# Kernel optimization log

Hardware: AMD Instinct MI355X
Metric: run time of the kernel (lower is better)

The kernel has to match this reference:

```python
import jax, jax.numpy as jnp
import numpy as np

N = 100000   # total nodes
E = 1000000  # edges
D = 64       # input_dim
H = 128      # embed_dim


def setup_inputs() -> dict:
    key = jax.random.key(0)
    k1, k2, k3, k4 = jax.random.split(key, 4)
    nodes = jnp.arange(N, dtype=jnp.int32)
    features = jax.random.normal(k1, (N, D), dtype=jnp.float32)
    edge_index = jax.random.randint(k2, (2, E), 0, N, dtype=jnp.int32)
    # nn.Linear(2*D, H): weight [H, 2D], bias [H]
    W = jax.random.normal(k3, (H, 2 * D), dtype=jnp.float32) / np.sqrt(2 * D)
    b = jax.random.normal(k4, (H,), dtype=jnp.float32) * 0.01
    return {"nodes": nodes, "features": features, "edge_index": edge_index,
            "W": W, "b": b}


def reference(nodes, features, edge_index, W, b):
    src, dst = edge_index[0], edge_index[1]
    # gcn=False: neighbors are undirected (both src->dst and dst->src).
    # Mean aggregator over all neighbors (full-neighborhood mean).
    ones = jnp.ones((E,), dtype=features.dtype)
    neigh_sum = (jax.ops.segment_sum(features[dst], src, num_segments=N)
                 + jax.ops.segment_sum(features[src], dst, num_segments=N))
    deg = (jax.ops.segment_sum(ones, src, num_segments=N)
           + jax.ops.segment_sum(ones, dst, num_segments=N))
    neigh_mean = neigh_sum / jnp.maximum(deg, 1.0)[:, None]  # [N, D]
    self_feats = features[nodes]            # [B, D]
    neigh_feats = neigh_mean[nodes]         # [B, D]
    combined = jnp.concatenate([self_feats, neigh_feats], axis=1)  # [B, 2D]
    out = jax.nn.relu(combined @ W.T + b)   # [B, H]
    return out
```

## Files before the change

### kernel.cpp

```cpp
#include <hip/hip_runtime.h>
#include <hip/hip_bf16.h>


#define D_IN 64
#define H_OUT 128
#define CAP 64
#define CAP_L 61
#define NPB 32
#define BSHIFT 8
#define BUK_N 256
#define NBUK_MAX 512
#define PASSA_BLOCKS 256
#define PASSA_THREADS 512

typedef unsigned long long ull;
typedef unsigned short ushortt;
typedef unsigned char uchar;
typedef __attribute__((ext_vector_type(8))) short bf16x8;
typedef __attribute__((ext_vector_type(4))) float f32x4;
typedef __attribute__((ext_vector_type(2))) float f32x2;

__device__ __forceinline__ ushortt f2bf(float f) {
    __hip_bfloat16 h = __float2bfloat16(f);
    return *reinterpret_cast<ushortt*>(&h);
}
__device__ __forceinline__ float bf2f(ushortt u) {
    unsigned int x = ((unsigned int)u) << 16;
    return __uint_as_float(x);
}

__global__ __launch_bounds__(PASSA_THREADS) void prep_kernel(
    const int* __restrict__ ei,
    unsigned* __restrict__ gbuf,
    int* __restrict__ blkcnt,
    const float4* __restrict__ feat4,
    const float4* __restrict__ w4,
    ushortt* __restrict__ fb,
    uint2* __restrict__ fq,
    ushortt* __restrict__ Wb,
    int E, int nbuk, int scap, int chunk, int nfeat8, int nw8)
{
    const int t = threadIdx.x;

    if (blockIdx.x >= PASSA_BLOCKS) {
        int i = (blockIdx.x - PASSA_BLOCKS) * PASSA_THREADS + t;
        if (i < nfeat8) {
            float4 a = feat4[2 * i], b = feat4[2 * i + 1];
            bf16x8 o;
            o[0] = (short)f2bf(a.x); o[1] = (short)f2bf(a.y);
            o[2] = (short)f2bf(a.z); o[3] = (short)f2bf(a.w);
            o[4] = (short)f2bf(b.x); o[5] = (short)f2bf(b.y);
            o[6] = (short)f2bf(b.z); o[7] = (short)f2bf(b.w);
            *(bf16x8*)&fb[(size_t)i * 8] = o;
            unsigned lo = (unsigned)__builtin_amdgcn_cvt_pk_fp8_f32(a.x, a.y, 0, false);
            lo = (unsigned)__builtin_amdgcn_cvt_pk_fp8_f32(a.z, a.w, (int)lo, true);
            unsigned hi = (unsigned)__builtin_amdgcn_cvt_pk_fp8_f32(b.x, b.y, 0, false);
            hi = (unsigned)__builtin_amdgcn_cvt_pk_fp8_f32(b.z, b.w, (int)hi, true);
            uint2 q; q.x = lo; q.y = hi;
            fq[i] = q;
        } else {
            int j = i - nfeat8;
            if (j < nw8) {
                float4 a = w4[2 * j], b = w4[2 * j + 1];
                bf16x8 o;
                o[0] = (short)f2bf(a.x); o[1] = (short)f2bf(a.y);
                o[2] = (short)f2bf(a.z); o[3] = (short)f2bf(a.w);
                o[4] = (short)f2bf(b.x); o[5] = (short)f2bf(b.y);
                o[6] = (short)f2bf(b.z); o[7] = (short)f2bf(b.w);
                *(bf16x8*)&Wb[(size_t)j * 8] = o;
            }
        }
        return;
    }

    __shared__ int lcnt[NBUK_MAX];
    for (int i = t; i < nbuk; i += PASSA_THREADS) lcnt[i] = 0;
    __syncthreads();

    const int E2 = 2 * E;
    int lo = blockIdx.x * chunk;
    int hi = lo + chunk; if (hi > E2) hi = E2;

    for (int i = lo + t; i < hi; i += PASSA_THREADS) {
        int u = ei[i];
        int v = (i < E) ? ei[E + i] : ei[i - E];
        int b = u >> BSHIFT;
        unsigned pk = ((unsigned)v << BSHIFT) | (unsigned)(u & (BUK_N - 1));
        int p = atomicAdd(&lcnt[b], 1);
        if (p < scap) gbuf[((size_t)blockIdx.x * nbuk + b) * scap + p] = pk;
    }
    __syncthreads();
    for (int b = t; b < nbuk; b += PASSA_THREADS)
        blkcnt[blockIdx.x * nbuk + b] = lcnt[b];
}

__global__ __launch_bounds__(1024) void adj_agg_kernel(
    const unsigned* __restrict__ gbuf,
    const int* __restrict__ blkcnt,
    const int* __restrict__ ei,
    const uchar* __restrict__ fq,
    ushortt* __restrict__ meanb,
    int N, int E, int nbuk, int scap)
{
    __shared__ unsigned adj_l[BUK_N * CAP_L];
    __shared__ int cnt_l[BUK_N];
    __shared__ int scnt_l[PASSA_BLOCKS];
    __shared__ int satf;

    const int b = blockIdx.x;
    const int t = threadIdx.x;

    if (t == 0) satf = 0;
    if (t < BUK_N) cnt_l[t] = 0;
    if (t < PASSA_BLOCKS) {
        int c = blkcnt[t * nbuk + b];
        scnt_l[t] = c;
        if (c > scap) satf = 1;
    }
    __syncthreads();

    const int wv   = t >> 6;
    const int lane = t & 63;

    if (satf) {
        const int E2 = 2 * E;
        for (int i = t; i < E2; i += 1024) {
            int u = ei[i];
            if ((u >> BSHIFT) != b) continue;
            int v = (i < E) ? ei[E + i] : ei[i - E];
            int ul = u & (BUK_N - 1);
            int p  = atomicAdd(&cnt_l[ul], 1);
            if (p < CAP_L) adj_l[ul * CAP_L + p] = (unsigned)v;
        }
    } else {
        for (int seg = wv; seg < PASSA_BLOCKS; seg += 16) {
            int c = scnt_l[seg]; if (c > scap) c = scap;
            const unsigned* base = gbuf + ((size_t)seg * nbuk + b) * scap;
            for (int i = lane; i < c; i += 64) {
                unsigned e = base[i];
                int ul = e & (BUK_N - 1);
                int v  = (int)(e >> BSHIFT);
                int p  = atomicAdd(&cnt_l[ul], 1);
                if (p < CAP_L) adj_l[ul * CAP_L + p] = (unsigned)v;
            }
        }
    }
    __syncthreads();

    const int oct = lane >> 3;
    const int ol  = lane & 7;
    const uchar* fqb = fq + ol * 8;

    const int nbase = wv * 16;
    const int gbase = (b << BSHIFT) + nbase;

#define GATH(U0, U1, U2, U3, AROW, CC)                                       \
    {                                                                        \
        if ((CC) > 0) {                                                      \
            int jj = oct;      int a = jj < (CC);                            \
            unsigned id = (AROW)[a ? jj : 0];                                \
            U0 = *(const uint2*)(fqb + (size_t)(id * 64u));                  \
            if (!a) { U0.x = 0u; U0.y = 0u; }                                \
        }                                                                    \
        if ((CC) > 8) {                                                      \
            int jj = 8 + oct;  int a = jj < (CC);                            \
            unsigned id = (AROW)[a ? jj : 0];                                \
            U1 = *(const uint2*)(fqb + (size_t)(id * 64u));                  \
            if (!a) { U1.x = 0u; U1.y = 0u; }                                \
        }                                                                    \
        if ((CC) > 16) {                                                     \
            int jj = 16 + oct; int a = jj < (CC);                            \
            unsigned id = (AROW)[a ? jj : 0];                                \
            U2 = *(const uint2*)(fqb + (size_t)(id * 64u));                  \
            if (!a) { U2.x = 0u; U2.y = 0u; }                                \
        }                                                                    \
        if ((CC) > 24) {                                                     \
            int jj = 24 + oct; int a = jj < (CC);                            \
            unsigned id = (AROW)[a ? jj : 0];                                \
            U3 = *(const uint2*)(fqb + (size_t)(id * 64u));                  \
            if (!a) { U3.x = 0u; U3.y = 0u; }                                \
        }                                                                    \
    }

#define DEC(u)                                                       \
    s0 += __builtin_amdgcn_cvt_pk_f32_fp8((int)(u).x, false);        \
    s1 += __builtin_amdgcn_cvt_pk_f32_fp8((int)(u).x, true);         \
    s2 += __builtin_amdgcn_cvt_pk_f32_fp8((int)(u).y, false);        \
    s3 += __builtin_amdgcn_cvt_pk_f32_fp8((int)(u).y, true);

#define FINISH(UA, UB, UC, UD, CC, CTRUE, AROW, G)                           \
    {                                                                        \
        f32x2 s0 = {0.f, 0.f}, s1 = {0.f, 0.f};                              \
        f32x2 s2 = {0.f, 0.f}, s3 = {0.f, 0.f};                              \
        DEC(UA); DEC(UB); DEC(UC); DEC(UD);                                  \
        if (__builtin_expect((CC) > 32, 0)) {                                \
            for (int j = 32; j < (CC); j += 8) {                             \
                int jj = j + oct; int a = jj < (CC);                         \
                unsigned id = (AROW)[a ? jj : 0];                            \
                uint2 u = *(const uint2*)(fqb + (size_t)(id * 64u));         \
                if (!a) { u.x = 0u; u.y = 0u; }                              \
                DEC(u);                                                      \
            }                                                                \
        }                                                                    \
        f32x2 a0, a1;                                                        \
        {                                                                    \
            f32x2 t0, t1, t2, t3;                                            \
            t0.x = __shfl_xor(s0.x, 8);  t0.y = __shfl_xor(s0.y, 8);         \
            t1.x = __shfl_xor(s1.x, 8);  t1.y = __shfl_xor(s1.y, 8);         \
            t2.x = __shfl_xor(s2.x, 8);  t2.y = __shfl_xor(s2.y, 8);         \
            t3.x = __shfl_xor(s3.x, 8);  t3.y = __shfl_xor(s3.y, 8);         \
            bool hi = (oct & 1);                                             \
            a0 = hi ? (s2 + t2) : (s0 + t0);                                 \
            a1 = hi ? (s3 + t3) : (s1 + t1);                                 \
        }                                                                    \
        f32x2 b0;                                                            \
        {                                                                    \
            f32x2 t0, t1;                                                    \
            t0.x = __shfl_xor(a0.x, 16); t0.y = __shfl_xor(a0.y, 16);        \
            t1.x = __shfl_xor(a1.x, 16); t1.y = __shfl_xor(a1.y, 16);        \
            bool hi = (oct & 2);                                             \
            b0 = hi ? (a1 + t1) : (a0 + t0);                                 \
        }                                                                    \
        float cf;                                                            \
        {                                                                    \
            f32x2 tt;                                                        \
            tt.x = __shfl_xor(b0.x, 32); tt.y = __shfl_xor(b0.y, 32);        \
            f32x2 ss = b0 + tt;                                              \
            cf = (oct & 4) ? ss.y : ss.x;                                    \
        }                                                                    \
        float r = 1.0f / fmaxf((float)(CTRUE), 1.0f);                        \
        int d = 8 * ol + 4 * (oct & 1) + (oct & 2) + ((oct >> 2) & 1);       \
        meanb[(size_t)(G) * D_IN + d] = f2bf(cf * r);                        \
    }

    for (int np = 0; np < 8; ++np) {
        const int n0 = nbase + 2 * np;
        const int g0 = gbase + 2 * np;
        const int g1 = g0 + 1;

        const int c0  = (g0 < N) ? cnt_l[n0] : 0;
        const int c1  = (g1 < N) ? cnt_l[n0 + 1] : 0;
        const int cc0 = c0 < CAP_L ? c0 : CAP_L;
        const int cc1 = c1 < CAP_L ? c1 : CAP_L;
        const unsigned* ar0 = &adj_l[n0 * CAP_L];
        const unsigned* ar1 = &adj_l[(n0 + 1) * CAP_L];

        uint2 u00 = {0u,0u}, u01 = {0u,0u}, u02 = {0u,0u}, u03 = {0u,0u};
        uint2 u10 = {0u,0u}, u11 = {0u,0u}, u12 = {0u,0u}, u13 = {0u,0u};
        GATH(u00, u01, u02, u03, ar0, cc0);
        GATH(u10, u11, u12, u13, ar1, cc1);

        if (g0 < N) FINISH(u00, u01, u02, u03, cc0, c0, ar0, g0);
        if (g1 < N) FINISH(u10, u11, u12, u13, cc1, c1, ar1, g1);
    }
#undef GATH
#undef DEC
#undef FINISH
}

__global__ __launch_bounds__(256) void build_adj_kernel(
    const int* __restrict__ ei,
    int* __restrict__ cnt,
    int* __restrict__ adj,
    int E)
{
    const int part   = blockIdx.x & 7;
    const int bloc   = blockIdx.x >> 3;
    const int nbp    = gridDim.x >> 3;
    const int stride = nbp * 256;
    const int E2     = 2 * E;

    for (int i = bloc * 256 + (int)threadIdx.x; i < E2; i += stride) {
        int u = ei[i];
        if (((u >> 4) & 7) != part) continue;
        int v = (i < E) ? ei[E + i] : ei[i - E];
        int p = atomicAdd(&cnt[u], 1);
        if (p < CAP_L) adj[u * CAP + p] = v;
    }
}

__global__ __launch_bounds__(256) void aggregate_f32_kernel(
    const float* __restrict__ feat,
    const int* __restrict__ adj,
    const int* __restrict__ cnt,
    ushortt* __restrict__ meanb,
    int N)
{
    int wid  = (blockIdx.x * blockDim.x + threadIdx.x) >> 6;
    int lane = threadIdx.x & 63;
    if (wid >= N) return;

    int c  = cnt[wid];
    int cc = c < CAP_L ? c : CAP_L;
    int ids = adj[wid * CAP + lane];

    float sum = 0.0f;
    int j = 0;
    for (; j + 8 <= cc; j += 8) {
        int i0 = __shfl(ids, j + 0);
        int i1 = __shfl(ids, j + 1);
        int i2 = __shfl(ids, j + 2);
        int i3 = __shfl(ids, j + 3);
        int i4 = __shfl(ids, j + 4);
        int i5 = __shfl(ids, j + 5);
        int i6 = __shfl(ids, j + 6);
        int i7 = __shfl(ids, j + 7);
        float f0 = feat[i0 * D_IN + lane];
        float f1 = feat[i1 * D_IN + lane];
        float f2 = feat[i2 * D_IN + lane];
        float f3 = feat[i3 * D_IN + lane];
        float f4 = feat[i4 * D_IN + lane];
        float f5 = feat[i5 * D_IN + lane];
        float f6 = feat[i6 * D_IN + lane];
        float f7 = feat[i7 * D_IN + lane];
        sum += ((f0 + f1) + (f2 + f3)) + ((f4 + f5) + (f6 + f7));
    }
    for (; j < cc; ++j)
        sum += feat[__shfl(ids, j) * D_IN + lane];

    float m = sum / fmaxf((float)c, 1.0f);
    meanb[(size_t)wid * D_IN + lane] = f2bf(m);
}

__global__ __launch_bounds__(256) void gemm_mfma_kernel(
    const int* __restrict__ nodes,
    const ushortt* __restrict__ fb,
    const ushortt* __restrict__ meanb,
    const ushortt* __restrict__ Wb,
    const float* __restrict__ bias,
    float* __restrict__ out,
    int N)
{
    __shared__ ushortt w_lds[128 * 136];
    __shared__ int gnode[64];

    const int t  = threadIdx.x;
    const int n0 = blockIdx.x * 64;

    if (t < 64) {
        int idx = n0 + t;
        gnode[t] = nodes[idx < N ? idx : N - 1];
    }
    for (int i = t; i < 128 * 16; i += 256) {
        int row = i >> 4, seg = i & 15;
        *(bf16x8*)&w_lds[row * 136 + seg * 8] =
            *(const bf16x8*)&Wb[row * 128 + seg * 8];
    }
    __syncthreads();

    const int w    = t >> 6;
    const int lane = t & 63;
    const int l15  = lane & 15;
    const int quad = lane >> 4;

    const int g = gnode[w * 16 + l15];
    const bf16x8 a0 = *(const bf16x8*)&fb[(size_t)g * D_IN +  0 + quad * 8];
    const bf16x8 a1 = *(const bf16x8*)&fb[(size_t)g * D_IN + 32 + quad * 8];
    const bf16x8 a2 = *(const bf16x8*)&meanb[(size_t)g * D_IN +  0 + quad * 8];
    const bf16x8 a3 = *(const bf16x8*)&meanb[(size_t)g * D_IN + 32 + quad * 8];

    const int  out_row = n0 + w * 16 + l15;
    const bool valid   = out_row < N;

#pragma unroll
    for (int tile = 0; tile < 8; ++tile) {
        const int h0 = tile * 16;
        const ushortt* wrow = &w_lds[(h0 + l15) * 136];
        bf16x8 b0 = *(const bf16x8*)&wrow[ 0 + quad * 8];
        bf16x8 b1 = *(const bf16x8*)&wrow[32 + quad * 8];
        bf16x8 b2 = *(const bf16x8*)&wrow[64 + quad * 8];
        bf16x8 b3 = *(const bf16x8*)&wrow[96 + quad * 8];

        f32x4 acc = {0.f, 0.f, 0.f, 0.f};
        acc = __builtin_amdgcn_mfma_f32_16x16x32_bf16(b0, a0, acc, 0, 0, 0);
        acc = __builtin_amdgcn_mfma_f32_16x16x32_bf16(b1, a1, acc, 0, 0, 0);
        acc = __builtin_amdgcn_mfma_f32_16x16x32_bf16(b2, a2, acc, 0, 0, 0);
        acc = __builtin_amdgcn_mfma_f32_16x16x32_bf16(b3, a3, acc, 0, 0, 0);

        if (valid) {
            float4 bv = *(const float4*)&bias[h0 + quad * 4];
            float4 o;
            o.x = fmaxf(acc[0] + bv.x, 0.0f);
            o.y = fmaxf(acc[1] + bv.y, 0.0f);
            o.z = fmaxf(acc[2] + bv.z, 0.0f);
            o.w = fmaxf(acc[3] + bv.w, 0.0f);
            *(float4*)&out[(size_t)out_row * H_OUT + h0 + quad * 4] = o;
        }
    }
}

__global__ __launch_bounds__(256) void gemm_kernel(
    const int* __restrict__ nodes,
    const float* __restrict__ feat,
    const ushortt* __restrict__ meanb,
    const float* __restrict__ W,
    const float* __restrict__ bias,
    float* __restrict__ out,
    int N)
{
    __shared__ float w_lds[64 * 132];
    __shared__ float comb_self[NPB * 68];
    __shared__ float comb_mean[NPB * 68];
    __shared__ int   gnode[NPB];

    const int t  = threadIdx.x;
    const int n0 = blockIdx.x * NPB;

    if (t < NPB) {
        int idx = n0 + t;
        if (idx >= N) idx = N - 1;
        gnode[t] = nodes[idx];
    }
    __syncthreads();

    for (int i = t; i < NPB * 64; i += 256) {
        int n = i >> 6, d = i & 63;
        int g = gnode[n];
        comb_self[n * 68 + d] = feat[g * D_IN + d];
        comb_mean[n * 68 + d] = bf2f(meanb[(size_t)g * D_IN + d]);
    }
    for (int i = t; i < H_OUT * 64; i += 256) {
        int h = i >> 6, kk = i & 63;
        w_lds[kk * 132 + h] = W[h * (2 * D_IN) + kk];
    }
    __syncthreads();

    const int tx = t & 31;
    const int ty = t >> 5;
    const int h0 = tx * 4;
    const int nl = ty * 4;

    float acc[4][4];
#pragma unroll
    for (int j = 0; j < 4; j++)
#pragma unroll
        for (int i = 0; i < 4; i++) acc[j][i] = 0.0f;

    for (int kk = 0; kk < 64; kk += 4) {
        float4 wvv[4], cv[4];
#pragma unroll
        for (int i = 0; i < 4; i++)
            wvv[i] = *(const float4*)&w_lds[(kk + i) * 132 + h0];
#pragma unroll
        for (int j = 0; j < 4; j++)
            cv[j] = *(const float4*)&comb_self[(nl + j) * 68 + kk];
#pragma unroll
        for (int j = 0; j < 4; j++) {
            const float* c = (const float*)&cv[j];
#pragma unroll
            for (int i = 0; i < 4; i++) {
                const float* wp = (const float*)&wvv[i];
                acc[j][0] += wp[0] * c[i];
                acc[j][1] += wp[1] * c[i];
                acc[j][2] += wp[2] * c[i];
                acc[j][3] += wp[3] * c[i];
            }
        }
    }
    __syncthreads();

    for (int i = t; i < H_OUT * 64; i += 256) {
        int h = i >> 6, kk = i & 63;
        w_lds[kk * 132 + h] = W[h * (2 * D_IN) + 64 + kk];
    }
    __syncthreads();

    for (int kk = 0; kk < 64; kk += 4) {
        float4 wvv[4], cv[4];
#pragma unroll
        for (int i = 0; i < 4; i++)
            wvv[i] = *(const float4*)&w_lds[(kk + i) * 132 + h0];
#pragma unroll
        for (int j = 0; j < 4; j++)
            cv[j] = *(const float4*)&comb_mean[(nl + j) * 68 + kk];
#pragma unroll
        for (int j = 0; j < 4; j++) {
            const float* c = (const float*)&cv[j];
#pragma unroll
            for (int i = 0; i < 4; i++) {
                const float* wp = (const float*)&wvv[i];
                acc[j][0] += wp[0] * c[i];
                acc[j][1] += wp[1] * c[i];
                acc[j][2] += wp[2] * c[i];
                acc[j][3] += wp[3] * c[i];
            }
        }
    }

    float4 bv = *(const float4*)&bias[h0];
#pragma unroll
    for (int j = 0; j < 4; j++) {
        int n = n0 + nl + j;
        if (n >= N) continue;
        float4 o;
        o.x = fmaxf(acc[j][0] + bv.x, 0.0f);
        o.y = fmaxf(acc[j][1] + bv.y, 0.0f);
        o.z = fmaxf(acc[j][2] + bv.z, 0.0f);
        o.w = fmaxf(acc[j][3] + bv.w, 0.0f);
        *(float4*)&out[(size_t)n * H_OUT + h0] = o;
    }
}

extern "C" void kernel_launch(void* const* d_in, const int* in_sizes, int n_in,
                              void* d_out, int out_size, void* d_ws, size_t ws_size,
                              hipStream_t stream) {
    const int*   nodes = (const int*)d_in[0];
    const float* feat  = (const float*)d_in[1];
    const int*   ei    = (const int*)d_in[2];
    const float* W     = (const float*)d_in[3];
    const float* bias  = (const float*)d_in[4];
    float*       out   = (float*)d_out;

    const int N  = in_sizes[0];
    const int E  = in_sizes[2] / 2;
    const int E2 = 2 * E;

    const int nbuk  = (N + BUK_N - 1) >> BSHIFT;
    const int chunk = (E2 + PASSA_BLOCKS - 1) / PASSA_BLOCKS;
    double ex = (double)chunk * (double)BUK_N / (double)N;
    int scap = ((int)(ex + 9.0 * __builtin_sqrt(ex)) + 31) & ~15;
    if (scap < 64) scap = 64;

    char* base = (char*)d_ws;
    size_t off = 0;
    auto aln = [](size_t x) { return (x + 63) & ~(size_t)63; };
    int*     cnt    = (int*)(base + off);     off = aln(off + (size_t)N * 4);
    int*     adj    = (int*)(base + off);     off = aln(off + (size_t)N * CAP * 4);
    ushortt* meanb  = (ushortt*)(base + off); off = aln(off + (size_t)N * D_IN * 2);
    int*     blkcnt = (int*)(base + off);     off = aln(off + (size_t)PASSA_BLOCKS * NBUK_MAX * 4);
    ushortt* Wb     = (ushortt*)(base + off); off = aln(off + (size_t)H_OUT * 2 * D_IN * 2);
    ushortt* fb     = (ushortt*)(base + off); off = aln(off + (size_t)N * D_IN * 2);
    uchar*   fq     = (uchar*)(base + off);   off = aln(off + (size_t)N * D_IN);
    unsigned* gbuf  = (unsigned*)(base + off);
    const size_t total = off + (size_t)PASSA_BLOCKS * nbuk * scap * 4;

    const bool full = (N <= 131072) && (nbuk <= NBUK_MAX) && (ws_size >= total)
                   && ((N * D_IN) % 8 == 0);

    if (full) {
        const int nfeat8 = N * D_IN / 8;
        const int nw8    = H_OUT * 2 * D_IN / 8;
        const int conv_blocks = (nfeat8 + nw8 + PASSA_THREADS - 1) / PASSA_THREADS;
        prep_kernel<<<PASSA_BLOCKS + conv_blocks, PASSA_THREADS, 0, stream>>>(
            ei, gbuf, blkcnt, (const float4*)feat, (const float4*)W,
            fb, (uint2*)fq, Wb, E, nbuk, scap, chunk, nfeat8, nw8);
        adj_agg_kernel<<<nbuk, 1024, 0, stream>>>(gbuf, blkcnt, ei, fq,
                                                  meanb, N, E, nbuk, scap);
        gemm_mfma_kernel<<<(N + 63) / 64, 256, 0, stream>>>(
            nodes, fb, meanb, Wb, bias, out, N);
    } else {
        const int ablocks = (int)(((size_t)N * 64 + 255) / 256);
        hipMemsetAsync(cnt, 0, (size_t)N * sizeof(int), stream);
        build_adj_kernel<<<2048, 256, 0, stream>>>(ei, cnt, adj, E);
        aggregate_f32_kernel<<<ablocks, 256, 0, stream>>>(feat, adj, cnt,
                                                          meanb, N);
        gemm_kernel<<<(N + NPB - 1) / NPB, 256, 0, stream>>>(
            nodes, feat, meanb, W, bias, out, N);
    }
}
```

Measured before the change: 169.9 us.

## Split fp8 feature table into two column halves and aggregate in two passes

The fp8 feature table is stored as two separate 32-byte-per-node tables, one per half of the feature columns. The aggregation kernel walks each node's neighbor list twice, once per half, so each pass touches a 3.2 MB table that fits better in cache during the random gathers. The cost is twice the LDS adjacency reads and index work, narrower 4-byte loads, and fewer bytes in flight per gather.

```diff
diff --git a/kernel.cpp b/kernel.cpp
--- a/kernel.cpp
+++ b/kernel.cpp
@@ -36,7 +36,8 @@
     const float4* __restrict__ feat4,
     const float4* __restrict__ w4,
     ushortt* __restrict__ fb,
-    uint2* __restrict__ fq,
+    uint2* __restrict__ fqA,
+    uint2* __restrict__ fqB,
     ushortt* __restrict__ Wb,
     int E, int nbuk, int scap, int chunk, int nfeat8, int nw8)
 {
@@ -57,7 +58,9 @@
             unsigned hi = (unsigned)__builtin_amdgcn_cvt_pk_fp8_f32(b.x, b.y, 0, false);
             hi = (unsigned)__builtin_amdgcn_cvt_pk_fp8_f32(b.z, b.w, (int)hi, true);
             uint2 q; q.x = lo; q.y = hi;
-            fq[i] = q;
+            int node = i >> 3, grp = i & 7;
+            if (grp < 4) fqA[node * 4 + grp]       = q;
+            else         fqB[node * 4 + (grp - 4)] = q;
         } else {
             int j = i - nfeat8;
             if (j < nw8) {
@@ -98,7 +101,8 @@
     const unsigned* __restrict__ gbuf,
     const int* __restrict__ blkcnt,
     const int* __restrict__ ei,
-    const uchar* __restrict__ fq,
+    const uchar* __restrict__ fqA,
+    const uchar* __restrict__ fqB,
     ushortt* __restrict__ meanb,
     int N, int E, int nbuk, int scap)
 {
@@ -149,109 +153,99 @@
 
     const int oct = lane >> 3;
     const int ol  = lane & 7;
-    const uchar* fqb = fq + ol * 8;
-
     const int nbase = wv * 16;
     const int gbase = (b << BSHIFT) + nbase;
 
-#define GATH(U0, U1, U2, U3, AROW, CC)                                       \
+#define GATH(U0, U1, U2, U3, AROW, CC, TBL)                                  \
     {                                                                        \
         if ((CC) > 0) {                                                      \
             int jj = oct;      int a = jj < (CC);                            \
             unsigned id = (AROW)[a ? jj : 0];                                \
-            U0 = *(const uint2*)(fqb + (size_t)(id * 64u));                  \
-            if (!a) { U0.x = 0u; U0.y = 0u; }                                \
+            U0 = *(const unsigned*)((TBL) + (size_t)(id * 32u) + ol * 4);    \
+            if (!a) U0 = 0u;                                                 \
         }                                                                    \
         if ((CC) > 8) {                                                      \
             int jj = 8 + oct;  int a = jj < (CC);                            \
             unsigned id = (AROW)[a ? jj : 0];                                \
-            U1 = *(const uint2*)(fqb + (size_t)(id * 64u));                  \
-            if (!a) { U1.x = 0u; U1.y = 0u; }                                \
+            U1 = *(const unsigned*)((TBL) + (size_t)(id * 32u) + ol * 4);    \
+            if (!a) U1 = 0u;                                                 \
         }                                                                    \
         if ((CC) > 16) {                                                     \
             int jj = 16 + oct; int a = jj < (CC);                            \
             unsigned id = (AROW)[a ? jj : 0];                                \
-            U2 = *(const uint2*)(fqb + (size_t)(id * 64u));                  \
-            if (!a) { U2.x = 0u; U2.y = 0u; }                                \
+            U2 = *(const unsigned*)((TBL) + (size_t)(id * 32u) + ol * 4);    \
+            if (!a) U2 = 0u;                                                 \
         }                                                                    \
         if ((CC) > 24) {                                                     \
             int jj = 24 + oct; int a = jj < (CC);                            \
             unsigned id = (AROW)[a ? jj : 0];                                \
-            U3 = *(const uint2*)(fqb + (size_t)(id * 64u));                  \
-            if (!a) { U3.x = 0u; U3.y = 0u; }                                \
+            U3 = *(const unsigned*)((TBL) + (size_t)(id * 32u) + ol * 4);    \
+            if (!a) U3 = 0u;                                                 \
         }                                                                    \
     }
 
 #define DEC(u)                                                       \
-    s0 += __builtin_amdgcn_cvt_pk_f32_fp8((int)(u).x, false);        \
-    s1 += __builtin_amdgcn_cvt_pk_f32_fp8((int)(u).x, true);         \
-    s2 += __builtin_amdgcn_cvt_pk_f32_fp8((int)(u).y, false);        \
-    s3 += __builtin_amdgcn_cvt_pk_f32_fp8((int)(u).y, true);
-
-#define FINISH(UA, UB, UC, UD, CC, CTRUE, AROW, G)                           \
+    s0 += __builtin_amdgcn_cvt_pk_f32_fp8((int)(u), false);          \
+    s1 += __builtin_amdgcn_cvt_pk_f32_fp8((int)(u), true);
+
+#define FINISH(UA, UB, UC, UD, CC, CTRUE, AROW, G, TBL, DBASE)               \
     {                                                                        \
         f32x2 s0 = {0.f, 0.f}, s1 = {0.f, 0.f};                              \
-        f32x2 s2 = {0.f, 0.f}, s3 = {0.f, 0.f};                              \
         DEC(UA); DEC(UB); DEC(UC); DEC(UD);                                  \
         if (__builtin_expect((CC) > 32, 0)) {                                \
             for (int j = 32; j < (CC); j += 8) {                             \
                 int jj = j + oct; int a = jj < (CC);                         \
                 unsigned id = (AROW)[a ? jj : 0];                            \
-                uint2 u = *(const uint2*)(fqb + (size_t)(id * 64u));         \
-                if (!a) { u.x = 0u; u.y = 0u; }                              \
+                unsigned u =                                                 \
+                    *(const unsigned*)((TBL) + (size_t)(id * 32u) + ol * 4); \
+                if (!a) u = 0u;                                              \
                 DEC(u);                                                      \
             }                                                                \
         }                                                                    \
-        f32x2 a0, a1;                                                        \
+        f32x2 a0;                                                            \
         {                                                                    \
-            f32x2 t0, t1, t2, t3;                                            \
+            f32x2 t0, t1;                                                    \
             t0.x = __shfl_xor(s0.x, 8);  t0.y = __shfl_xor(s0.y, 8);         \
             t1.x = __shfl_xor(s1.x, 8);  t1.y = __shfl_xor(s1.y, 8);         \
-            t2.x = __shfl_xor(s2.x, 8);  t2.y = __shfl_xor(s2.y, 8);         \
-            t3.x = __shfl_xor(s3.x, 8);  t3.y = __shfl_xor(s3.y, 8);         \
-            bool hi = (oct & 1);                                             \
-            a0 = hi ? (s2 + t2) : (s0 + t0);                                 \
-            a1 = hi ? (s3 + t3) : (s1 + t1);                                 \
-        }                                                                    \
-        f32x2 b0;                                                            \
-        {                                                                    \
-            f32x2 t0, t1;                                                    \
-            t0.x = __shfl_xor(a0.x, 16); t0.y = __shfl_xor(a0.y, 16);        \
-            t1.x = __shfl_xor(a1.x, 16); t1.y = __shfl_xor(a1.y, 16);        \
-            bool hi = (oct & 2);                                             \
-            b0 = hi ? (a1 + t1) : (a0 + t0);                                 \
-        }                                                                    \
-        float cf;                                                            \
-        {                                                                    \
-            f32x2 tt;                                                        \
-            tt.x = __shfl_xor(b0.x, 32); tt.y = __shfl_xor(b0.y, 32);        \
-            f32x2 ss = b0 + tt;                                              \
-            cf = (oct & 4) ? ss.y : ss.x;                                    \
-        }                                                                    \
-        float r = 1.0f / fmaxf((float)(CTRUE), 1.0f);                        \
-        int d = 8 * ol + 4 * (oct & 1) + (oct & 2) + ((oct >> 2) & 1);       \
-        meanb[(size_t)(G) * D_IN + d] = f2bf(cf * r);                        \
-    }
-
-    for (int np = 0; np < 8; ++np) {
-        const int n0 = nbase + 2 * np;
-        const int g0 = gbase + 2 * np;
-        const int g1 = g0 + 1;
-
-        const int c0  = (g0 < N) ? cnt_l[n0] : 0;
-        const int c1  = (g1 < N) ? cnt_l[n0 + 1] : 0;
-        const int cc0 = c0 < CAP_L ? c0 : CAP_L;
-        const int cc1 = c1 < CAP_L ? c1 : CAP_L;
-        const unsigned* ar0 = &adj_l[n0 * CAP_L];
-        const unsigned* ar1 = &adj_l[(n0 + 1) * CAP_L];
-
-        uint2 u00 = {0u,0u}, u01 = {0u,0u}, u02 = {0u,0u}, u03 = {0u,0u};
-        uint2 u10 = {0u,0u}, u11 = {0u,0u}, u12 = {0u,0u}, u13 = {0u,0u};
-        GATH(u00, u01, u02, u03, ar0, cc0);
-        GATH(u10, u11, u12, u13, ar1, cc1);
-
-        if (g0 < N) FINISH(u00, u01, u02, u03, cc0, c0, ar0, g0);
-        if (g1 < N) FINISH(u10, u11, u12, u13, cc1, c1, ar1, g1);
+            a0 = (oct & 1) ? (s1 + t1) : (s0 + t0);                          \
+        }                                                                    \
+        { f32x2 tt; tt.x = __shfl_xor(a0.x, 16); tt.y = __shfl_xor(a0.y, 16);\
+          a0 += tt; }                                                        \
+        { f32x2 tt; tt.x = __shfl_xor(a0.x, 32); tt.y = __shfl_xor(a0.y, 32);\
+          a0 += tt; }                                                        \
+        if (oct < 2) {                                                       \
+            float r = 1.0f / fmaxf((float)(CTRUE), 1.0f);                    \
+            int d = 4 * ol + 2 * oct;                                        \
+            unsigned o = (unsigned)f2bf(a0.x * r)                            \
+                       | ((unsigned)f2bf(a0.y * r) << 16);                   \
+            *(unsigned*)&meanb[(size_t)(G) * D_IN + (DBASE) + d] = o;        \
+        }                                                                    \
+    }
+
+    for (int pass = 0; pass < 2; ++pass) {
+        const uchar* tbl = pass ? fqB : fqA;
+        const int dbase  = pass << 5;
+
+        for (int np = 0; np < 8; ++np) {
+            const int n0 = nbase + 2 * np;
+            const int g0 = gbase + 2 * np;
+            const int g1 = g0 + 1;
+
+            const int c0  = (g0 < N) ? cnt_l[n0] : 0;
+            const int c1  = (g1 < N) ? cnt_l[n0 + 1] : 0;
+            const int cc0 = c0 < CAP_L ? c0 : CAP_L;
+            const int cc1 = c1 < CAP_L ? c1 : CAP_L;
+            const unsigned* ar0 = &adj_l[n0 * CAP_L];
+            const unsigned* ar1 = &adj_l[(n0 + 1) * CAP_L];
+
+            unsigned u00 = 0u, u01 = 0u, u02 = 0u, u03 = 0u;
+            unsigned u10 = 0u, u11 = 0u, u12 = 0u, u13 = 0u;
+            GATH(u00, u01, u02, u03, ar0, cc0, tbl);
+            GATH(u10, u11, u12, u13, ar1, cc1, tbl);
+
+            if (g0 < N) FINISH(u00, u01, u02, u03, cc0, c0, ar0, g0, tbl, dbase);
+            if (g1 < N) FINISH(u10, u11, u12, u13, cc1, c1, ar1, g1, tbl, dbase);
+        }
     }
 #undef GATH
 #undef DEC
@@ -530,7 +524,8 @@
     int*     blkcnt = (int*)(base + off);     off = aln(off + (size_t)PASSA_BLOCKS * NBUK_MAX * 4);
     ushortt* Wb     = (ushortt*)(base + off); off = aln(off + (size_t)H_OUT * 2 * D_IN * 2);
     ushortt* fb     = (ushortt*)(base + off); off = aln(off + (size_t)N * D_IN * 2);
-    uchar*   fq     = (uchar*)(base + off);   off = aln(off + (size_t)N * D_IN);
+    uchar*   fqA    = (uchar*)(base + off);   off = aln(off + (size_t)N * 32);
+    uchar*   fqB    = (uchar*)(base + off);   off = aln(off + (size_t)N * 32);
     unsigned* gbuf  = (unsigned*)(base + off);
     const size_t total = off + (size_t)PASSA_BLOCKS * nbuk * scap * 4;
 
@@ -543,8 +538,9 @@
         const int conv_blocks = (nfeat8 + nw8 + PASSA_THREADS - 1) / PASSA_THREADS;
         prep_kernel<<<PASSA_BLOCKS + conv_blocks, PASSA_THREADS, 0, stream>>>(
             ei, gbuf, blkcnt, (const float4*)feat, (const float4*)W,
-            fb, (uint2*)fq, Wb, E, nbuk, scap, chunk, nfeat8, nw8);
-        adj_agg_kernel<<<nbuk, 1024, 0, stream>>>(gbuf, blkcnt, ei, fq,
+            fb, (uint2*)fqA, (uint2*)fqB, Wb, E, nbuk, scap, chunk,
+            nfeat8, nw8);
+        adj_agg_kernel<<<nbuk, 1024, 0, stream>>>(gbuf, blkcnt, ei, fqA, fqB,
                                                   meanb, N, E, nbuk, scap);
         gemm_mfma_kernel<<<(N + 63) / 64, 256, 0, stream>>>(
             nodes, fb, meanb, Wb, bias, out, N);
```

Result: slower. 185.5 us (+9.2%).
